# Kernel optimization log

Hardware: AMD Instinct MI355X
Metric: run time of the kernel (lower is better)

## Reference

```python
import jax, jax.numpy as jnp
import numpy as np

BLANK = 59  # CFG['pad_phrase'] == blank_index == label pad value
NEG = jnp.float32(-1e30)  # -inf surrogate safe for logaddexp


def setup_inputs() -> dict:
    key = jax.random.key(0)
    k1, k2 = jax.random.split(key)
    B, T, V, L = 1024, 384, 60, 45
    labels = jax.random.randint(k1, (B, L), 0, BLANK, dtype=jnp.int32)
    logits = jax.random.normal(k2, (B, T, V), dtype=jnp.float32)
    return {"labels": labels, "logits": logits}


def _ctc_loss(logits, labels):
    # logits: [B, T, V] (not time-major), labels: [B, L] padded with BLANK
    B, T, V = logits.shape
    L = labels.shape[1]
    S = 2 * L + 1  # extended label length: blanks interleaved

    logp = jax.nn.log_softmax(logits, axis=-1)  # tf.nn.ctc_loss softmaxes internally

    # extended label sequence: [blank, l1, blank, l2, ..., blank]
    ext = jnp.full((B, S), BLANK, dtype=jnp.int32).at[:, 1::2].set(labels)
    # per-step emission log-probs for each extended-label position: [B, T, S]
    emit = jnp.take_along_axis(logp, ext[:, None, :], axis=2)

    # skip transition s-2 -> s allowed iff s >= 2, ext[s] != blank, ext[s] != ext[s-2]
    ext_m2 = jnp.pad(ext[:, :-2], ((0, 0), (2, 0)), constant_values=-1)
    skip_ok = (jnp.arange(S) >= 2) & (ext != BLANK) & (ext != ext_m2)

    # alpha init at t=0: only positions 0 (blank) and 1 (first label) reachable
    alpha0 = jnp.full((B, S), NEG).at[:, 0].set(emit[:, 0, 0]).at[:, 1].set(emit[:, 0, 1])

    def step(alpha, emit_t):
        s1 = jnp.pad(alpha[:, :-1], ((0, 0), (1, 0)), constant_values=NEG)
        s2 = jnp.where(skip_ok, jnp.pad(alpha[:, :-2], ((0, 0), (2, 0)), constant_values=NEG), NEG)
        alpha = jnp.logaddexp(jnp.logaddexp(alpha, s1), s2) + emit_t
        return alpha, None

    emit_tbs = jnp.swapaxes(emit, 0, 1)  # [T, B, S]
    alpha_T, _ = jax.lax.scan(step, alpha0, emit_tbs[1:])

    # label_length = number of non-pad tokens (as in the TF layer)
    label_len = jnp.sum((labels != BLANK).astype(jnp.int32), axis=-1)
    end = 2 * label_len  # index of final blank in extended sequence
    a_blank = jnp.take_along_axis(alpha_T, end[:, None], axis=1)[:, 0]
    a_label = jnp.take_along_axis(alpha_T, jnp.maximum(end - 1, 0)[:, None], axis=1)[:, 0]
    a_label = jnp.where(end > 0, a_label, NEG)
    nll = -jnp.logaddexp(a_blank, a_label)  # [B]
    return jnp.mean(nll)


def reference(labels, logits):
    return _ctc_loss(logits, labels)
```

## Files before the change

kernel.cpp:

```cpp
#include <hip/hip_runtime.h>
#include <hip/hip_fp16.h>

#define BLANKC 59

typedef _Float16 half8 __attribute__((ext_vector_type(8)));
typedef _Float16 half4 __attribute__((ext_vector_type(4)));

#define LDS_FENCE() asm volatile("s_waitcnt lgkmcnt(0)" ::: "memory")

__device__ __forceinline__ float wave_shr1(float x, float fill) {
    int r = __builtin_amdgcn_update_dpp(__float_as_int(fill), __float_as_int(x),
                                        0x138 , 0xF, 0xF, false);
    return __int_as_float(r);
}

template <int CTRL>
__device__ __forceinline__ float dpp_fmax(float x) {
    int r = __builtin_amdgcn_update_dpp(__float_as_int(x), __float_as_int(x),
                                        CTRL, 0xF, 0xF, false);
    return fmaxf(x, __int_as_float(r));
}

template <int CTRL>
__device__ __forceinline__ float dpp_addf(float x) {
    int r = __builtin_amdgcn_update_dpp(__float_as_int(x), __float_as_int(x),
                                        CTRL, 0xF, 0xF, false);
    return x + __int_as_float(r);
}

__device__ __forceinline__ float wave_max_bcast(float x) {
    x = dpp_fmax<0x111>(x);
    x = dpp_fmax<0x112>(x);
    x = dpp_fmax<0x114>(x);
    x = dpp_fmax<0x118>(x);
    x = dpp_fmax<0x142>(x);
    x = dpp_fmax<0x143>(x);
    return __int_as_float(__builtin_amdgcn_readlane(__float_as_int(x), 63));
}

#define RS   392
#define NCH  48
#define SCRS 68

__global__ __launch_bounds__(256)
void ctc_fused(const int* __restrict__ labels, const float* __restrict__ logits,
               float* __restrict__ out, int T, int V, int L, float inv_b) {
    const int b    = blockIdx.x;
    const int tid  = threadIdx.x;
    const int lane = tid & 63;
    const int wid  = tid >> 6;

    __shared__ __align__(16) __half S[46 * RS];
    __shared__ __align__(16) __half scr[3][8][SCRS];
    __shared__ int labs[64];
    __shared__ int flags[4];

    if (tid < 64) labs[tid] = (tid < L) ? labels[(long)b * L + tid] : BLANKC;
    if (tid < 4)  flags[tid] = 0;
    __syncthreads();

    if (wid != 0) {
        const int w  = wid - 1;
        const int tq = lane >> 3;
        const int q  = lane & 7;
        const int c0 = q * 8;
        const bool full = (q < 7);
        const float* src = logits + (long)b * T * V;

        int gl[6], gr[6], gv[6]; bool gok[6];
        #pragma unroll
        for (int k = 0; k < 6; ++k) {
            const int i = lane + (k << 6);
            gok[k] = (i < 368);
            gl[k] = i >> 3; gr[k] = i & 7;
            const int ll = gok[k] ? gl[k] : 0;
            gv[k] = (ll < 45) ? labs[ll] : BLANKC;
        }

        float4 A0, A1{0.f,0.f,0.f,0.f}, B0{0.f,0.f,0.f,0.f}, B1;
        {   const float* p = src + (w * 128 + tq) * 60 + c0;
            A0 = *(const float4*)p;
            if (full) A1 = *(const float4*)(p + 4);
        }
        for (int pass = 0; pass < 16; ++pass) {
            const int tbase = w * 128 + pass * 8;
            B1 = float4{0.f,0.f,0.f,0.f};
            if (pass < 15) {
                const float* p = src + (tbase + 8 + tq) * 60 + c0;
                B0 = *(const float4*)p;
                if (full) B1 = *(const float4*)(p + 4);
            }
            const float e0 = __expf(A0.x), e1 = __expf(A0.y),
                        e2 = __expf(A0.z), e3 = __expf(A0.w);
            float e4 = 0.f, e5 = 0.f, e6 = 0.f, e7 = 0.f;
            if (full) { e4 = __expf(A1.x); e5 = __expf(A1.y);
                        e6 = __expf(A1.z); e7 = __expf(A1.w); }
            float s = ((e0 + e1) + (e2 + e3)) + ((e4 + e5) + (e6 + e7));
            s = dpp_addf<0xB1>(s);
            s = dpp_addf<0x4E>(s);
            s += __shfl_xor(s, 4, 64);
            const float inv = __builtin_amdgcn_rcpf(s);
            const half4 p0 = { (_Float16)(e0 * inv), (_Float16)(e1 * inv),
                               (_Float16)(e2 * inv), (_Float16)(e3 * inv) };
            const half4 p1 = { (_Float16)(e4 * inv), (_Float16)(e5 * inv),
                               (_Float16)(e6 * inv), (_Float16)(e7 * inv) };
            *(half4*)&scr[w][tq][c0]     = p0;
            *(half4*)&scr[w][tq][c0 + 4] = p1;
            LDS_FENCE();

            const int c = tbase >> 3;
            #pragma unroll
            for (int k = 0; k < 6; ++k) {
                if (gok[k]) {
                    const int cp = c ^ ((gl[k] >> 3) & 7);
                    S[gl[k] * RS + cp * 8 + gr[k]] = scr[w][gr[k]][gv[k]];
                }
            }
            LDS_FENCE();
            if (lane == 0)
                __hip_atomic_fetch_add(&flags[w], 1, __ATOMIC_RELAXED,
                                       __HIP_MEMORY_SCOPE_WORKGROUP);
            A0 = B0; A1 = B1;
        }
        return;
    }

    const int labL = (lane < L) ? labs[lane] : BLANKC;
    const int labP = (lane >= 1 && lane < L) ? labs[lane - 1] : BLANKC;
    const float skipf = ((lane >= 1) && (lane < L) && (labL != BLANKC) && (labL != labP))
                        ? 1.0f : 0.0f;
    const unsigned long long mk = __ballot((lane < L) && (labL != BLANKC));
    const int len = __popcll(mk);

    const int rl = (lane < 45) ? lane : 45;
    const __half* baseL = &S[rl * RS];
    const __half* baseB = &S[45 * RS];
    const int xL = (rl >> 3) & 7;
    const int xB = 5;

    float a0 = 0.f, a1 = 0.f;
    int esum = 0;

    auto step = [&](float eL, float eB) {
        const float p   = wave_shr1(a1, 0.0f);
        const float t1  = a0 + a1;
        const float na0 = (a0 + p) * eB;
        const float na1 = fmaf(skipf, p, t1) * eL;
        a0 = na0; a1 = na1;
    };
    auto renorm = [&]() {
        const float m = wave_max_bcast(fmaxf(a0, a1));
        const int e = (__float_as_int(m) >> 23) & 0xff;
        int sexp = 207 - e;
        if (sexp > 127) sexp = 127;
        const float sc = __int_as_float((sexp + 127) << 23);
        a0 *= sc; a1 *= sc;
        esum += sexp;
    };

    int seen = 0, curw = -1;
    auto waitc = [&](int c) {
        const int w = c >> 4, pw = c & 15;
        if (w != curw) {
            curw = w;
            seen = __hip_atomic_load(&flags[w], __ATOMIC_RELAXED,
                                     __HIP_MEMORY_SCOPE_WORKGROUP);
        }
        while (seen <= pw) {
            __builtin_amdgcn_s_sleep(2);
            seen = __hip_atomic_load(&flags[curw], __ATOMIC_RELAXED,
                                     __HIP_MEMORY_SCOPE_WORKGROUP);
        }
        asm volatile("" ::: "memory");
    };
    const half8 hz = {};
    auto loadch = [&](int c, half8& hL, half8& hB) {
        hL = *(const half8*)(baseL + (c ^ xL) * 8);
        hB = *(const half8*)(baseB + (c ^ xB) * 8);
        if (lane >= 45) hL = hz;
        if (lane >= 46) hB = hz;
    };

    half8 cL, cB, nL, nB;
    waitc(0);
    loadch(0, cL, cB);
    for (int c = 0; c < NCH; ++c) {
        if (c + 1 < NCH) { waitc(c + 1); loadch(c + 1, nL, nB); }
        if (c == 0) {
            a0 = (lane == 0) ? (float)cB[0] * 0x1p80f : 0.f;
            a1 = (lane == 0) ? (float)cL[0] * 0x1p80f : 0.f;
            esum = 80;
            #pragma unroll
            for (int i = 1; i < 8; ++i) step((float)cL[i], (float)cB[i]);
        } else {
            #pragma unroll
            for (int i = 0; i < 8; ++i) step((float)cL[i], (float)cB[i]);
        }
        renorm();
        cL = nL; cB = nB;
    }

    const float ab2 = __shfl(a0, len, 64);
    float al2 = __shfl(a1, (len > 0) ? len - 1 : 0, 64);
    al2 = (len > 0) ? al2 : 0.f;
    if (lane == 0) {
        const float s   = ab2 + al2;
        const float nll = -(__logf(s) - (float)esum * 0.69314718056f);
        atomicAdd(out, nll * inv_b);
    }
}

extern "C" void kernel_launch(void* const* d_in, const int* in_sizes, int n_in,
                              void* d_out, int out_size, void* d_ws, size_t ws_size,
                              hipStream_t stream) {
    const int* labels   = (const int*)d_in[0];
    const float* logits = (const float*)d_in[1];
    float* out          = (float*)d_out;
    (void)d_ws; (void)ws_size;

    const int L = 45, V = 60;
    const int B = in_sizes[0] / L;
    const int T = in_sizes[1] / (B * V);

    hipMemsetAsync(out, 0, (size_t)out_size * sizeof(float), stream);
    ctc_fused<<<B, 256, 0, stream>>>(labels, logits, out, T, V, L, 1.0f / (float)B);
}
```

Baseline: 159.7 us.

## Split CTC recursion into concurrent forward and backward waves meeting at midpoint

Instead of one wave running the full alpha recursion over all 48 time chunks, wave 0 runs the forward alpha pass over the first 24 chunks while wave 1 runs a backward beta pass from the last chunk down to chunk 24. Two producer waves fill the emission table from both ends to match. At the midpoint the two waves combine alpha and beta in log2 space with a wave-wide max and sum. This roughly halves the serial dependent chain per block. In exchange it drops one producer wave and adds a combine step, an extra wait flag and some precision risk from mixing alpha and beta at a single time step.

Result: faster. 154.8 us (-3.1%).

```diff
diff --git a/kernel.cpp b/kernel.cpp
--- a/kernel.cpp
+++ b/kernel.cpp
@@ -11,6 +11,11 @@
 __device__ __forceinline__ float wave_shr1(float x, float fill) {
     int r = __builtin_amdgcn_update_dpp(__float_as_int(fill), __float_as_int(x),
                                         0x138 , 0xF, 0xF, false);
+    return __int_as_float(r);
+}
+__device__ __forceinline__ float wave_shl1(float x, float fill) {
+    int r = __builtin_amdgcn_update_dpp(__float_as_int(fill), __float_as_int(x),
+                                        0x130 , 0xF, 0xF, false);
     return __int_as_float(r);
 }
 
@@ -20,26 +25,26 @@
                                         CTRL, 0xF, 0xF, false);
     return fmaxf(x, __int_as_float(r));
 }
-
 template <int CTRL>
 __device__ __forceinline__ float dpp_addf(float x) {
     int r = __builtin_amdgcn_update_dpp(__float_as_int(x), __float_as_int(x),
                                         CTRL, 0xF, 0xF, false);
     return x + __int_as_float(r);
 }
-
 __device__ __forceinline__ float wave_max_bcast(float x) {
-    x = dpp_fmax<0x111>(x);
-    x = dpp_fmax<0x112>(x);
-    x = dpp_fmax<0x114>(x);
-    x = dpp_fmax<0x118>(x);
-    x = dpp_fmax<0x142>(x);
-    x = dpp_fmax<0x143>(x);
+    x = dpp_fmax<0x111>(x); x = dpp_fmax<0x112>(x);
+    x = dpp_fmax<0x114>(x); x = dpp_fmax<0x118>(x);
+    x = dpp_fmax<0x142>(x); x = dpp_fmax<0x143>(x);
     return __int_as_float(__builtin_amdgcn_readlane(__float_as_int(x), 63));
 }
+__device__ __forceinline__ float wave_sum_bcast(float x) {
+    x = dpp_addf<0x111>(x); x = dpp_addf<0x112>(x);
+    x = dpp_addf<0x114>(x); x = dpp_addf<0x118>(x);
+    x = dpp_addf<0x142>(x); x = dpp_addf<0x143>(x);
+    return __int_as_float(__builtin_amdgcn_readlane(__float_as_int(x), 63));
+}
 
 #define RS   392
-#define NCH  48
 #define SCRS 68
 
 __global__ __launch_bounds__(256)
@@ -51,16 +56,18 @@
     const int wid  = tid >> 6;
 
     __shared__ __align__(16) __half S[46 * RS];
-    __shared__ __align__(16) __half scr[3][8][SCRS];
+    __shared__ __align__(16) __half scr[2][8][SCRS];
+    __shared__ float fa0[64], fa1[64];
     __shared__ int labs[64];
-    __shared__ int flags[4];
+    __shared__ int flags[2];
+    __shared__ int esF_s, wdone;
 
     if (tid < 64) labs[tid] = (tid < L) ? labels[(long)b * L + tid] : BLANKC;
-    if (tid < 4)  flags[tid] = 0;
+    if (tid == 0) { flags[0] = 0; flags[1] = 0; wdone = 0; }
     __syncthreads();
 
-    if (wid != 0) {
-        const int w  = wid - 1;
+    if (wid >= 2) {
+        const int h  = wid - 2;
         const int tq = lane >> 3;
         const int q  = lane & 7;
         const int c0 = q * 8;
@@ -78,15 +85,17 @@
         }
 
         float4 A0, A1{0.f,0.f,0.f,0.f}, B0{0.f,0.f,0.f,0.f}, B1;
-        {   const float* p = src + (w * 128 + tq) * 60 + c0;
+        {   const int ch0 = h ? 47 : 0;
+            const float* p = src + (ch0 * 8 + tq) * 60 + c0;
             A0 = *(const float4*)p;
             if (full) A1 = *(const float4*)(p + 4);
         }
-        for (int pass = 0; pass < 16; ++pass) {
-            const int tbase = w * 128 + pass * 8;
+        for (int pass = 0; pass < 24; ++pass) {
+            const int ch = h ? (47 - pass) : pass;
             B1 = float4{0.f,0.f,0.f,0.f};
-            if (pass < 15) {
-                const float* p = src + (tbase + 8 + tq) * 60 + c0;
+            if (pass < 23) {
+                const int ch2 = h ? (46 - pass) : (pass + 1);
+                const float* p = src + (ch2 * 8 + tq) * 60 + c0;
                 B0 = *(const float4*)p;
                 if (full) B1 = *(const float4*)(p + 4);
             }
@@ -104,21 +113,20 @@
                                (_Float16)(e2 * inv), (_Float16)(e3 * inv) };
             const half4 p1 = { (_Float16)(e4 * inv), (_Float16)(e5 * inv),
                                (_Float16)(e6 * inv), (_Float16)(e7 * inv) };
-            *(half4*)&scr[w][tq][c0]     = p0;
-            *(half4*)&scr[w][tq][c0 + 4] = p1;
+            *(half4*)&scr[h][tq][c0]     = p0;
+            *(half4*)&scr[h][tq][c0 + 4] = p1;
             LDS_FENCE();
 
-            const int c = tbase >> 3;
             #pragma unroll
             for (int k = 0; k < 6; ++k) {
                 if (gok[k]) {
-                    const int cp = c ^ ((gl[k] >> 3) & 7);
-                    S[gl[k] * RS + cp * 8 + gr[k]] = scr[w][gr[k]][gv[k]];
+                    const int cp = ch ^ ((gl[k] >> 3) & 7);
+                    S[gl[k] * RS + cp * 8 + gr[k]] = scr[h][gr[k]][gv[k]];
                 }
             }
             LDS_FENCE();
             if (lane == 0)
-                __hip_atomic_fetch_add(&flags[w], 1, __ATOMIC_RELAXED,
+                __hip_atomic_fetch_add(&flags[h], 1, __ATOMIC_RELAXED,
                                        __HIP_MEMORY_SCOPE_WORKGROUP);
             A0 = B0; A1 = B1;
         }
@@ -138,41 +146,6 @@
     const int xL = (rl >> 3) & 7;
     const int xB = 5;
 
-    float a0 = 0.f, a1 = 0.f;
-    int esum = 0;
-
-    auto step = [&](float eL, float eB) {
-        const float p   = wave_shr1(a1, 0.0f);
-        const float t1  = a0 + a1;
-        const float na0 = (a0 + p) * eB;
-        const float na1 = fmaf(skipf, p, t1) * eL;
-        a0 = na0; a1 = na1;
-    };
-    auto renorm = [&]() {
-        const float m = wave_max_bcast(fmaxf(a0, a1));
-        const int e = (__float_as_int(m) >> 23) & 0xff;
-        int sexp = 207 - e;
-        if (sexp > 127) sexp = 127;
-        const float sc = __int_as_float((sexp + 127) << 23);
-        a0 *= sc; a1 *= sc;
-        esum += sexp;
-    };
-
-    int seen = 0, curw = -1;
-    auto waitc = [&](int c) {
-        const int w = c >> 4, pw = c & 15;
-        if (w != curw) {
-            curw = w;
-            seen = __hip_atomic_load(&flags[w], __ATOMIC_RELAXED,
-                                     __HIP_MEMORY_SCOPE_WORKGROUP);
-        }
-        while (seen <= pw) {
-            __builtin_amdgcn_s_sleep(2);
-            seen = __hip_atomic_load(&flags[curw], __ATOMIC_RELAXED,
-                                     __HIP_MEMORY_SCOPE_WORKGROUP);
-        }
-        asm volatile("" ::: "memory");
-    };
     const half8 hz = {};
     auto loadch = [&](int c, half8& hL, half8& hB) {
         hL = *(const half8*)(baseL + (c ^ xL) * 8);
@@ -181,31 +154,104 @@
         if (lane >= 46) hB = hz;
     };
 
+    const int h = wid;
+    int seen = 0;
+    auto waitp = [&](int need) {
+        while (seen < need) {
+            __builtin_amdgcn_s_sleep(1);
+            seen = __hip_atomic_load(&flags[h], __ATOMIC_RELAXED,
+                                     __HIP_MEMORY_SCOPE_WORKGROUP);
+        }
+        asm volatile("" ::: "memory");
+    };
+
+    if (wid == 0) {
+        float a0 = 0.f, a1 = 0.f;
+        int esum = 80;
+        auto step = [&](float eL, float eB) {
+            const float p   = wave_shr1(a1, 0.0f);
+            const float t1  = a0 + a1;
+            const float na0 = (a0 + p) * eB;
+            const float na1 = fmaf(skipf, p, t1) * eL;
+            a0 = na0; a1 = na1;
+        };
+        auto renorm = [&]() {
+            const float m = wave_max_bcast(fmaxf(a0, a1));
+            const int e = (__float_as_int(m) >> 23) & 0xff;
+            int sexp = 207 - e;
+            if (sexp > 127) sexp = 127;
+            const float sc = __int_as_float((sexp + 127) << 23);
+            a0 *= sc; a1 *= sc;
+            esum += sexp;
+        };
+        half8 cL, cB, nL, nB;
+        waitp(1); loadch(0, cL, cB);
+        for (int c = 0; c < 24; ++c) {
+            if (c + 1 < 24) { waitp(c + 2); loadch(c + 1, nL, nB); }
+            if (c == 0) {
+                a0 = (lane == 0) ? (float)cB[0] * 0x1p80f : 0.f;
+                a1 = (lane == 0) ? (float)cL[0] * 0x1p80f : 0.f;
+                #pragma unroll
+                for (int i = 1; i < 8; ++i) step((float)cL[i], (float)cB[i]);
+            } else {
+                #pragma unroll
+                for (int i = 0; i < 8; ++i) step((float)cL[i], (float)cB[i]);
+            }
+            renorm();
+            cL = nL; cB = nB;
+        }
+        fa0[lane] = a0;
+        fa1[lane] = a1;
+        if (lane == 0) esF_s = esum;
+        LDS_FENCE();
+        if (lane == 0)
+            __hip_atomic_store(&wdone, 1, __ATOMIC_RELAXED,
+                               __HIP_MEMORY_SCOPE_WORKGROUP);
+        return;
+    }
+
+    float g0 = (lane == len) ? 0x1p80f : 0.f;
+    float g1 = (lane == len - 1) ? 0x1p80f : 0.f;
+    int esum = 80;
+    auto bstep = [&](float eL, float eB) {
+        const float h0 = g0 * eB;
+        const float h1 = g1 * eL;
+        const float qq = wave_shl1(fmaf(skipf, h1, h0), 0.0f);
+        g0 = h0 + h1;
+        g1 = h1 + qq;
+    };
+    auto renormB = [&]() {
+        const float m = wave_max_bcast(fmaxf(g0, g1));
+        const int e = (__float_as_int(m) >> 23) & 0xff;
+        int sexp = 207 - e;
+        if (sexp > 127) sexp = 127;
+        const float sc = __int_as_float((sexp + 127) << 23);
+        g0 *= sc; g1 *= sc;
+        esum += sexp;
+    };
     half8 cL, cB, nL, nB;
-    waitc(0);
-    loadch(0, cL, cB);
-    for (int c = 0; c < NCH; ++c) {
-        if (c + 1 < NCH) { waitc(c + 1); loadch(c + 1, nL, nB); }
-        if (c == 0) {
-            a0 = (lane == 0) ? (float)cB[0] * 0x1p80f : 0.f;
-            a1 = (lane == 0) ? (float)cL[0] * 0x1p80f : 0.f;
-            esum = 80;
-            #pragma unroll
-            for (int i = 1; i < 8; ++i) step((float)cL[i], (float)cB[i]);
-        } else {
-            #pragma unroll
-            for (int i = 0; i < 8; ++i) step((float)cL[i], (float)cB[i]);
-        }
-        renorm();
+    waitp(1); loadch(47, cL, cB);
+    for (int k = 0; k < 24; ++k) {
+        if (k + 1 < 24) { waitp(k + 2); loadch(46 - k, nL, nB); }
+        #pragma unroll
+        for (int i = 7; i >= 0; --i) bstep((float)cL[i], (float)cB[i]);
+        renormB();
         cL = nL; cB = nB;
     }
 
-    const float ab2 = __shfl(a0, len, 64);
-    float al2 = __shfl(a1, (len > 0) ? len - 1 : 0, 64);
-    al2 = (len > 0) ? al2 : 0.f;
+    int d = __hip_atomic_load(&wdone, __ATOMIC_RELAXED, __HIP_MEMORY_SCOPE_WORKGROUP);
+    while (!d) {
+        __builtin_amdgcn_s_sleep(1);
+        d = __hip_atomic_load(&wdone, __ATOMIC_RELAXED, __HIP_MEMORY_SCOPE_WORKGROUP);
+    }
+    asm volatile("" ::: "memory");
+    const float t0 = __log2f(fa0[lane]) + __log2f(g0);
+    const float t1 = __log2f(fa1[lane]) + __log2f(g1);
+    const float m  = wave_max_bcast(fmaxf(t0, t1));
+    const float tt = wave_sum_bcast(exp2f(t0 - m) + exp2f(t1 - m));
     if (lane == 0) {
-        const float s   = ab2 + al2;
-        const float nll = -(__logf(s) - (float)esum * 0.69314718056f);
+        const float log2P = m + __log2f(tt) - (float)(esum + esF_s);
+        const float nll = -0.69314718055994531f * log2P;
         atomicAdd(out, nll * inv_b);
     }
 }
```
